# Kernel tuning notes

Measured on AMD Instinct MI355X. Metric: run time of the kernel, lower is better.

Reference implementation:

```python
import jax, jax.numpy as jnp
import numpy as np

B, C, H, W = 64, 128, 32, 32
GROUPS = 32
EPS = 1e-6
SCALE = 0.044194173824159216  # 1/sqrt(512), as hardcoded in the torch module


def setup_inputs() -> dict:
    key = jax.random.key(0)
    ks = jax.random.split(key, 12)
    s = 1.0 / np.sqrt(C)
    return {
        "x": jax.random.normal(ks[0], (B, C, H, W), dtype=jnp.float32),
        "gn_w": jax.random.normal(ks[1], (C,), dtype=jnp.float32) * 0.02 + 1.0,
        "gn_b": jax.random.normal(ks[2], (C,), dtype=jnp.float32) * 0.02,
        "wq": jax.random.uniform(ks[3], (C, C), jnp.float32, -s, s),
        "bq": jax.random.uniform(ks[4], (C,), jnp.float32, -s, s),
        "wk": jax.random.uniform(ks[5], (C, C), jnp.float32, -s, s),
        "bk": jax.random.uniform(ks[6], (C,), jnp.float32, -s, s),
        "wv": jax.random.uniform(ks[7], (C, C), jnp.float32, -s, s),
        "bv": jax.random.uniform(ks[8], (C,), jnp.float32, -s, s),
        "wo": jax.random.uniform(ks[9], (C, C), jnp.float32, -s, s),
        "bo": jax.random.uniform(ks[10], (C,), jnp.float32, -s, s),
    }


def reference(x, gn_w, gn_b, wq, bq, wk, bk, wv, bv, wo, bo):
    b = x.shape[0]
    res = x
    # GroupNorm(32 groups, 128 channels): normalize over (channels_per_group, H, W)
    xg = x.reshape(b, GROUPS, C // GROUPS, H * W)
    mean = xg.mean(axis=(2, 3), keepdims=True)
    var = xg.var(axis=(2, 3), keepdims=True)
    xn = (xg - mean) * jax.lax.rsqrt(var + EPS)
    xn = xn.reshape(b, C, H, W) * gn_w[:, None, None] + gn_b[:, None, None]
    # flatten spatial -> sequence: [b, S=1024, C=128]
    t = xn.reshape(b, C, H * W).transpose(0, 2, 1)
    q = t @ wq.T + bq
    k = t @ wk.T + bk
    v = t @ wv.T + bv
    att = jnp.einsum('bsc,btc->bst', q, k) * SCALE  # [b, S, S]
    att = jax.nn.softmax(att, axis=-1)
    o = jnp.einsum('bst,btc->bsc', att, v)
    o = o @ wo.T + bo
    out = o.transpose(0, 2, 1).reshape(b, C, H, W) + res
    return out
```

## Files before the change

kernel.cpp:

```cpp
#include <hip/hip_runtime.h>
#include <hip/hip_bf16.h>

#define BATCH 64
#define CCH 128
#define SEQ 1024
#define NG 32
#define EPSV 1e-6f
#define SCALEV 0.044194173824159216f

typedef short v8s __attribute__((ext_vector_type(8)));
typedef short v4s __attribute__((ext_vector_type(4)));
typedef float v4f __attribute__((ext_vector_type(4)));
typedef unsigned short us;

__device__ __forceinline__ us f2bf(float f) {
    __hip_bfloat16 h = __float2bfloat16(f);
    return *reinterpret_cast<us*>(&h);
}

#define MFMA16(a, b, c) __builtin_amdgcn_mfma_f32_16x16x32_bf16(a, b, c, 0, 0, 0)

__device__ __forceinline__ void gld_lds16(const us* g, us* l) {
    __builtin_amdgcn_global_load_lds(
        (const __attribute__((address_space(1))) void*)g,
        (__attribute__((address_space(3))) void*)l, 16, 0, 0);
}

__global__ void prep_gn(const float* __restrict__ wq, const float* __restrict__ wk,
                        const float* __restrict__ wv, const float* __restrict__ wo,
                        us* wbf, const float* __restrict__ x,
                        float* meanr, float* rstdr) {
    int tid = threadIdx.x;
    if (blockIdx.x < 256) {
        int i = blockIdx.x * 256 + tid;
        const float* srcs[4] = {wq, wk, wv, wo};
        wbf[i] = f2bf(srcs[i >> 14][i & 16383]);
        return;
    }
    int bg = blockIdx.x - 256;
    const float4* p = (const float4*)(x + (size_t)bg * (4 * SEQ));
    float s1 = 0.f, s2 = 0.f;
    #pragma unroll
    for (int i = 0; i < 4; i++) {
        float4 v = p[i * 256 + tid];
        s1 += v.x + v.y + v.z + v.w;
        s2 += v.x * v.x + v.y * v.y + v.z * v.z + v.w * v.w;
    }
    #pragma unroll
    for (int off = 32; off; off >>= 1) {
        s1 += __shfl_down(s1, off);
        s2 += __shfl_down(s2, off);
    }
    __shared__ float a1[4], a2[4];
    int w = tid >> 6, l = tid & 63;
    if (l == 0) { a1[w] = s1; a2[w] = s2; }
    __syncthreads();
    if (tid == 0) {
        float t1 = a1[0] + a1[1] + a1[2] + a1[3];
        float t2 = a2[0] + a2[1] + a2[2] + a2[3];
        float mean = t1 * (1.0f / (4 * SEQ));
        float var  = t2 * (1.0f / (4 * SEQ)) - mean * mean;
        meanr[bg] = mean;
        rstdr[bg] = rsqrtf(var + EPSV);
    }
}

__global__ __launch_bounds__(256, 2) void qkv_kernel(
    const float* __restrict__ x, const float* __restrict__ gn_w,
    const float* __restrict__ gn_b, const float* __restrict__ meanr,
    const float* __restrict__ rstdr, const us* __restrict__ wbf,
    const float* __restrict__ bq, const float* __restrict__ bk,
    const float* __restrict__ bv,
    us* Q, us* K, us* Vt)
{
    __shared__ us tls[64 * 136];
    int b  = blockIdx.x >> 4;
    int s0 = (blockIdx.x & 15) * 64;
    int tid = threadIdx.x;
    const float* xb = x + (size_t)b * CCH * SEQ;

    for (int rep = 0; rep < 32; rep++) {
        int idx = rep * 256 + tid;
        int c = idx >> 6, s = idx & 63;
        float v = xb[c * SEQ + s0 + s];
        int g = c >> 2;
        float t = (v - meanr[b * NG + g]) * rstdr[b * NG + g] * gn_w[c] + gn_b[c];
        tls[s * 136 + c] = f2bf(t);
    }
    __syncthreads();

    int w = tid >> 6, lane = tid & 63;
    int m = lane & 15, quad = lane >> 4;

    v8s bfr[6][4];
    float bias[6];
    #pragma unroll
    for (int t = 0; t < 6; t++) {
        int T = w * 6 + t;
        int o = T >> 3, ct = T & 7;
        const us* wmat = wbf + o * 16384;
        #pragma unroll
        for (int ch = 0; ch < 4; ch++)
            bfr[t][ch] = *(const v8s*)&wmat[(ct * 16 + m) * 128 + ch * 32 + quad * 8];
        const float* bb = (o == 0) ? bq : (o == 1) ? bk : bv;
        bias[t] = bb[ct * 16 + m];
    }

    us* Qb = Q + (size_t)b * SEQ * CCH;
    us* Kb = K + (size_t)b * SEQ * CCH;
    us* Vb = Vt + (size_t)b * CCH * SEQ;

    #pragma unroll
    for (int st = 0; st < 4; st++) {
        v8s a[4];
        #pragma unroll
        for (int ch = 0; ch < 4; ch++)
            a[ch] = *(const v8s*)&tls[(st * 16 + m) * 136 + ch * 32 + quad * 8];
        int srow = s0 + st * 16 + quad * 4;
        #pragma unroll
        for (int t = 0; t < 6; t++) {
            int T = w * 6 + t;
            int o = T >> 3, ct = T & 7;
            v4f acc = {0,0,0,0};
            #pragma unroll
            for (int ch = 0; ch < 4; ch++)
                acc = MFMA16(a[ch], bfr[t][ch], acc);
            int col = ct * 16 + m;
            if (o < 2) {
                us* dst = (o == 0) ? Qb : Kb;
                #pragma unroll
                for (int r = 0; r < 4; r++)
                    dst[(size_t)(srow + r) * 128 + col] = f2bf(acc[r] + bias[t]);
            } else {
                v4s pk;
                #pragma unroll
                for (int r = 0; r < 4; r++) pk[r] = (short)f2bf(acc[r] + bias[t]);
                *(v4s*)&Vb[(size_t)col * SEQ + srow] = pk;
            }
        }
    }
}

__global__ __launch_bounds__(256, 3) void attn_kernel(
    const us* __restrict__ Q, const us* __restrict__ K,
    const us* __restrict__ Vt, const us* __restrict__ wbo,
    const float* __restrict__ bo, const float* __restrict__ x,
    float* __restrict__ out)
{
    __shared__ char smem_raw[51200];
    us* klds = (us*)smem_raw;
    us* vlds = (us*)(smem_raw + 16384);
    us* plds = (us*)(smem_raw + 32768);
    us* olds = (us*)smem_raw;

    int i = blockIdx.x;
    int b  = (i & 7) * 8 + ((i >> 3) & 7);
    int qt = i >> 6;
    int tid = threadIdx.x;
    int w = tid >> 6, lane = tid & 63;
    int m = lane & 15, quad = lane >> 4;
    int qrow0 = qt * 128 + w * 32;
    const us* Qb = Q + (size_t)b * SEQ * CCH;
    const us* Kb = K + (size_t)b * SEQ * CCH;
    const us* Vb = Vt + (size_t)b * CCH * SEQ;
    us* pw = plds + w * 32 * 72;

    v8s aq[2][4];
    #pragma unroll
    for (int st = 0; st < 2; st++)
        #pragma unroll
        for (int ch = 0; ch < 4; ch++)
            aq[st][ch] = *(const v8s*)&Qb[(size_t)(qrow0 + st * 16 + m) * 128 + ch * 32 + quad * 8];

    v4f oacc[2][8];
    #pragma unroll
    for (int st = 0; st < 2; st++)
        #pragma unroll
        for (int ct = 0; ct < 8; ct++) oacc[st][ct] = (v4f){0, 0, 0, 0};
    float lrun[2][4] = {{0.f,0.f,0.f,0.f},{0.f,0.f,0.f,0.f}};

    const us* kg[4]; const us* vg[4];
    #pragma unroll
    for (int j4 = 0; j4 < 4; j4++) {
        int j = w * 4 + j4;
        int kr = 4 * j + (lane >> 4);
        kg[j4] = Kb + (size_t)kr * 128 + ((lane & 15) ^ (kr & 15)) * 8;
        int vc = 8 * j + (lane >> 3);
        vg[j4] = Vb + (size_t)vc * SEQ + ((lane & 7) ^ (vc & 7)) * 8;
    }

    for (int kt = 0; kt < 16; kt++) {
        __syncthreads();
        #pragma unroll
        for (int j4 = 0; j4 < 4; j4++) {
            int j = w * 4 + j4;
            gld_lds16(kg[j4] + kt * 8192, klds + j * 512);
            gld_lds16(vg[j4] + kt * 64,   vlds + j * 512);
        }
        __syncthreads();

        #pragma unroll
        for (int c2 = 0; c2 < 4; c2++) {
            int krow = c2 * 16 + m;
            v4f acc0 = {0,0,0,0}, acc1 = {0,0,0,0};
            #pragma unroll
            for (int ch = 0; ch < 4; ch++) {
                int chunk = (ch * 4 + quad) ^ (krow & 15);
                v8s kb = *(const v8s*)&klds[krow * 128 + chunk * 8];
                acc0 = MFMA16(aq[0][ch], kb, acc0);
                acc1 = MFMA16(aq[1][ch], kb, acc1);
            }
            #pragma unroll
            for (int r = 0; r < 4; r++) {
                float p0 = __expf(acc0[r] * SCALEV);
                float p1 = __expf(acc1[r] * SCALEV);
                lrun[0][r] += p0;
                lrun[1][r] += p1;
                pw[(quad * 4 + r) * 72 + c2 * 16 + m]      = f2bf(p0);
                pw[(16 + quad * 4 + r) * 72 + c2 * 16 + m] = f2bf(p1);
            }
        }
        v8s pa[2][2];
        #pragma unroll
        for (int st = 0; st < 2; st++)
            #pragma unroll
            for (int kc2 = 0; kc2 < 2; kc2++)
                pa[st][kc2] = *(const v8s*)&pw[(st * 16 + m) * 72 + kc2 * 32 + quad * 8];
        #pragma unroll
        for (int ct = 0; ct < 8; ct++) {
            int vrow = ct * 16 + m;
            #pragma unroll
            for (int kc2 = 0; kc2 < 2; kc2++) {
                int chunk = (kc2 * 4 + quad) ^ (vrow & 7);
                v8s vb = *(const v8s*)&vlds[vrow * 64 + chunk * 8];
                oacc[0][ct] = MFMA16(pa[0][kc2], vb, oacc[0][ct]);
                oacc[1][ct] = MFMA16(pa[1][kc2], vb, oacc[1][ct]);
            }
        }
    }
    float inv[2][4];
    #pragma unroll
    for (int st = 0; st < 2; st++)
        #pragma unroll
        for (int r = 0; r < 4; r++) {
            float rs = lrun[st][r];
            rs += __shfl_xor(rs, 1);
            rs += __shfl_xor(rs, 2);
            rs += __shfl_xor(rs, 4);
            rs += __shfl_xor(rs, 8);
            inv[st][r] = 1.0f / rs;
        }
    __syncthreads();
    #pragma unroll
    for (int st = 0; st < 2; st++)
        #pragma unroll
        for (int ct = 0; ct < 8; ct++)
            #pragma unroll
            for (int r = 0; r < 4; r++)
                olds[(w * 32 + st * 16 + quad * 4 + r) * 136 + ct * 16 + m] =
                    f2bf(oacc[st][ct][r] * inv[st][r]);
    __syncthreads();
    const float* xb = x + (size_t)b * CCH * SEQ;
    float* ob = out + (size_t)b * CCH * SEQ;
    int sbase = qt * 128 + w * 32;
    v8s obf[2][4];
    #pragma unroll
    for (int st = 0; st < 2; st++)
        #pragma unroll
        for (int ch = 0; ch < 4; ch++)
            obf[st][ch] = *(const v8s*)&olds[(w * 32 + st * 16 + m) * 136 + ch * 32 + quad * 8];
    #pragma unroll
    for (int mt = 0; mt < 8; mt++) {
        v8s af[4];
        #pragma unroll
        for (int ch = 0; ch < 4; ch++)
            af[ch] = *(const v8s*)&wbo[(mt * 16 + m) * 128 + ch * 32 + quad * 8];
        #pragma unroll
        for (int st = 0; st < 2; st++) {
            v4f acc = {0,0,0,0};
            #pragma unroll
            for (int ch = 0; ch < 4; ch++)
                acc = MFMA16(af[ch], obf[st][ch], acc);
            #pragma unroll
            for (int r = 0; r < 4; r++) {
                int c = mt * 16 + quad * 4 + r;
                int idx = c * SEQ + sbase + st * 16 + m;
                ob[idx] = acc[r] + bo[c] + xb[idx];
            }
        }
    }
}

extern "C" void kernel_launch(void* const* d_in, const int* in_sizes, int n_in,
                              void* d_out, int out_size, void* d_ws, size_t ws_size,
                              hipStream_t stream) {
    const float* x    = (const float*)d_in[0];
    const float* gn_w = (const float*)d_in[1];
    const float* gn_b = (const float*)d_in[2];
    const float* wq   = (const float*)d_in[3];
    const float* bq   = (const float*)d_in[4];
    const float* wk   = (const float*)d_in[5];
    const float* bk   = (const float*)d_in[6];
    const float* wv   = (const float*)d_in[7];
    const float* bv   = (const float*)d_in[8];
    const float* wo   = (const float*)d_in[9];
    const float* bo   = (const float*)d_in[10];
    float* out = (float*)d_out;

    char* ws = (char*)d_ws;
    us* wbf      = (us*)ws;
    float* meanr = (float*)(ws + 131072);
    float* rstdr = (float*)(ws + 139264);
    us* Qbuf     = (us*)(ws + 147456);
    us* Kbuf     = (us*)(ws + 147456 + 16777216ull);
    us* Vtbuf    = (us*)(ws + 147456 + 2ull * 16777216ull);

    prep_gn<<<256 + BATCH * NG, 256, 0, stream>>>(wq, wk, wv, wo, wbf, x, meanr, rstdr);
    qkv_kernel<<<1024, 256, 0, stream>>>(x, gn_w, gn_b, meanr, rstdr, wbf,
                                         bq, bk, bv, Qbuf, Kbuf, Vtbuf);
    attn_kernel<<<512, 256, 0, stream>>>(Qbuf, Kbuf, Vtbuf, wbf + 3 * 16384,
                                         bo, x, out);
}
```

Baseline: 192.0 us.

## Keep softmax probabilities in registers via transposed MFMA and lane shuffles

The QK^T MFMA now takes K as the A operand, so each lane holds score columns that can be packed to bf16 and redistributed with lane shuffles into the PV A-operand layout. This removes the per-tile LDS store and reload of P along with the P scratch region. Row sums are reduced across quads to match the new layout. The attention kernel also shrinks to 128-thread blocks covering 64 query rows, launched as 1024 blocks. That gives smaller LDS use and a looser register bound, but each block re-streams the full K and V for half as many queries.

```diff
diff --git a/kernel.cpp b/kernel.cpp
--- a/kernel.cpp
+++ b/kernel.cpp
@@ -11,6 +11,7 @@
 typedef short v8s __attribute__((ext_vector_type(8)));
 typedef short v4s __attribute__((ext_vector_type(4)));
 typedef float v4f __attribute__((ext_vector_type(4)));
+typedef int   v4i __attribute__((ext_vector_type(4)));
 typedef unsigned short us;
 
 __device__ __forceinline__ us f2bf(float f) {
@@ -141,16 +142,15 @@
     }
 }
 
-__global__ __launch_bounds__(256, 3) void attn_kernel(
+__global__ __launch_bounds__(128, 2) void attn_kernel(
     const us* __restrict__ Q, const us* __restrict__ K,
     const us* __restrict__ Vt, const us* __restrict__ wbo,
     const float* __restrict__ bo, const float* __restrict__ x,
     float* __restrict__ out)
 {
-    __shared__ char smem_raw[51200];
+    __shared__ char smem_raw[32768];
     us* klds = (us*)smem_raw;
     us* vlds = (us*)(smem_raw + 16384);
-    us* plds = (us*)(smem_raw + 32768);
     us* olds = (us*)smem_raw;
 
     int i = blockIdx.x;
@@ -159,11 +159,10 @@
     int tid = threadIdx.x;
     int w = tid >> 6, lane = tid & 63;
     int m = lane & 15, quad = lane >> 4;
-    int qrow0 = qt * 128 + w * 32;
+    int qrow0 = qt * 64 + w * 32;
     const us* Qb = Q + (size_t)b * SEQ * CCH;
     const us* Kb = K + (size_t)b * SEQ * CCH;
     const us* Vb = Vt + (size_t)b * CCH * SEQ;
-    us* pw = plds + w * 32 * 72;
 
     v8s aq[2][4];
     #pragma unroll
@@ -177,28 +176,31 @@
     for (int st = 0; st < 2; st++)
         #pragma unroll
         for (int ct = 0; ct < 8; ct++) oacc[st][ct] = (v4f){0, 0, 0, 0};
-    float lrun[2][4] = {{0.f,0.f,0.f,0.f},{0.f,0.f,0.f,0.f}};
-
-    const us* kg[4]; const us* vg[4];
-    #pragma unroll
-    for (int j4 = 0; j4 < 4; j4++) {
-        int j = w * 4 + j4;
+    float lrun[2] = {0.f, 0.f};
+
+    const us* kg[8]; const us* vg[8];
+    #pragma unroll
+    for (int j8 = 0; j8 < 8; j8++) {
+        int j = w * 8 + j8;
         int kr = 4 * j + (lane >> 4);
-        kg[j4] = Kb + (size_t)kr * 128 + ((lane & 15) ^ (kr & 15)) * 8;
+        kg[j8] = Kb + (size_t)kr * 128 + ((lane & 15) ^ (kr & 15)) * 8;
         int vc = 8 * j + (lane >> 3);
-        vg[j4] = Vb + (size_t)vc * SEQ + ((lane & 7) ^ (vc & 7)) * 8;
-    }
+        vg[j8] = Vb + (size_t)vc * SEQ + ((lane & 7) ^ (vc & 7)) * 8;
+    }
+    int idx0 = 2 * (quad & 1) * 16 + m;
+    int idx1 = idx0 + 16;
 
     for (int kt = 0; kt < 16; kt++) {
         __syncthreads();
         #pragma unroll
-        for (int j4 = 0; j4 < 4; j4++) {
-            int j = w * 4 + j4;
-            gld_lds16(kg[j4] + kt * 8192, klds + j * 512);
-            gld_lds16(vg[j4] + kt * 64,   vlds + j * 512);
+        for (int j8 = 0; j8 < 8; j8++) {
+            int j = w * 8 + j8;
+            gld_lds16(kg[j8] + kt * 8192, klds + j * 512);
+            gld_lds16(vg[j8] + kt * 64,   vlds + j * 512);
         }
         __syncthreads();
 
+        int e[2][4][2];
         #pragma unroll
         for (int c2 = 0; c2 < 4; c2++) {
             int krow = c2 * 16 + m;
@@ -207,25 +209,36 @@
             for (int ch = 0; ch < 4; ch++) {
                 int chunk = (ch * 4 + quad) ^ (krow & 15);
                 v8s kb = *(const v8s*)&klds[krow * 128 + chunk * 8];
-                acc0 = MFMA16(aq[0][ch], kb, acc0);
-                acc1 = MFMA16(aq[1][ch], kb, acc1);
-            }
+                acc0 = MFMA16(kb, aq[0][ch], acc0);
+                acc1 = MFMA16(kb, aq[1][ch], acc1);
+            }
+            float p0[4], p1[4];
             #pragma unroll
             for (int r = 0; r < 4; r++) {
-                float p0 = __expf(acc0[r] * SCALEV);
-                float p1 = __expf(acc1[r] * SCALEV);
-                lrun[0][r] += p0;
-                lrun[1][r] += p1;
-                pw[(quad * 4 + r) * 72 + c2 * 16 + m]      = f2bf(p0);
-                pw[(16 + quad * 4 + r) * 72 + c2 * 16 + m] = f2bf(p1);
-            }
+                p0[r] = __expf(acc0[r] * SCALEV);
+                p1[r] = __expf(acc1[r] * SCALEV);
+                lrun[0] += p0[r];
+                lrun[1] += p1[r];
+            }
+            e[0][c2][0] = (int)f2bf(p0[0]) | ((int)f2bf(p0[1]) << 16);
+            e[0][c2][1] = (int)f2bf(p0[2]) | ((int)f2bf(p0[3]) << 16);
+            e[1][c2][0] = (int)f2bf(p1[0]) | ((int)f2bf(p1[1]) << 16);
+            e[1][c2][1] = (int)f2bf(p1[2]) | ((int)f2bf(p1[3]) << 16);
         }
         v8s pa[2][2];
         #pragma unroll
         for (int st = 0; st < 2; st++)
             #pragma unroll
-            for (int kc2 = 0; kc2 < 2; kc2++)
-                pa[st][kc2] = *(const v8s*)&pw[(st * 16 + m) * 72 + kc2 * 32 + quad * 8];
+            for (int kc2 = 0; kc2 < 2; kc2++) {
+                int c0 = (quad < 2) ? e[st][2 * kc2][0] : e[st][2 * kc2 + 1][0];
+                int c1 = (quad < 2) ? e[st][2 * kc2][1] : e[st][2 * kc2 + 1][1];
+                v4i t;
+                t[0] = __shfl(c0, idx0);
+                t[1] = __shfl(c1, idx0);
+                t[2] = __shfl(c0, idx1);
+                t[3] = __shfl(c1, idx1);
+                pa[st][kc2] = __builtin_bit_cast(v8s, t);
+            }
         #pragma unroll
         for (int ct = 0; ct < 8; ct++) {
             int vrow = ct * 16 + m;
@@ -240,16 +253,14 @@
     }
     float inv[2][4];
     #pragma unroll
-    for (int st = 0; st < 2; st++)
-        #pragma unroll
-        for (int r = 0; r < 4; r++) {
-            float rs = lrun[st][r];
-            rs += __shfl_xor(rs, 1);
-            rs += __shfl_xor(rs, 2);
-            rs += __shfl_xor(rs, 4);
-            rs += __shfl_xor(rs, 8);
-            inv[st][r] = 1.0f / rs;
-        }
+    for (int st = 0; st < 2; st++) {
+        float rs = lrun[st];
+        rs += __shfl_xor(rs, 16);
+        rs += __shfl_xor(rs, 32);
+        #pragma unroll
+        for (int r = 0; r < 4; r++)
+            inv[st][r] = 1.0f / __shfl(rs, quad * 4 + r);
+    }
     __syncthreads();
     #pragma unroll
     for (int st = 0; st < 2; st++)
@@ -262,7 +273,7 @@
     __syncthreads();
     const float* xb = x + (size_t)b * CCH * SEQ;
     float* ob = out + (size_t)b * CCH * SEQ;
-    int sbase = qt * 128 + w * 32;
+    int sbase = qt * 64 + w * 32;
     v8s obf[2][4];
     #pragma unroll
     for (int st = 0; st < 2; st++)
@@ -318,6 +329,6 @@
     prep_gn<<<256 + BATCH * NG, 256, 0, stream>>>(wq, wk, wv, wo, wbf, x, meanr, rstdr);
     qkv_kernel<<<1024, 256, 0, stream>>>(x, gn_w, gn_b, meanr, rstdr, wbf,
                                          bq, bk, bv, Qbuf, Kbuf, Vtbuf);
-    attn_kernel<<<512, 256, 0, stream>>>(Qbuf, Kbuf, Vtbuf, wbf + 3 * 16384,
-                                         bo, x, out);
-}
+    attn_kernel<<<1024, 128, 0, stream>>>(Qbuf, Kbuf, Vtbuf, wbf + 3 * 16384,
+                                          bo, x, out);
+}
```

Measured after the change: 181.0 us. -5.7%, faster.
